# Kernel optimization log

Hardware: AMD Instinct MI355X
Metric: run time of the kernel (lower is better)

Reference implementation:

```python
import jax, jax.numpy as jnp
import numpy as np

EPS = 1e-7  # K.epsilon()
ROUTINGS = 3


def squash(v, axis=-1):
    s2 = jnp.sum(jnp.square(v), axis=axis, keepdims=True)
    scale = s2 / (1.0 + s2) / jnp.sqrt(s2 + EPS)
    return scale * v


def setup_inputs() -> dict:
    key = jax.random.key(0)
    kx, kw = jax.random.split(key)
    B, In, Din, Nc, Dc = 64, 2048, 16, 32, 32
    x = jax.random.normal(kx, (B, In, Din), dtype=jnp.float32)
    W = jax.random.normal(kw, (Nc, In, Dc, Din), dtype=jnp.float32) * 0.05
    return {"x": x, "W": W}


def reference(x, W):
    # x: [B, In, Din]; W: [Nc, In, Dc, Din]
    # Prediction vectors u_hat[b,i,j,d] = sum_k W[j,i,d,k] * x[b,i,k]
    # (the original tf.scan over batch + batch_dot computes exactly this,
    #  serialized; here it is a single batched einsum)
    hat = jnp.einsum('bik,jidk->bijd', x, W)  # [B, In, Nc, Dc]
    b = jnp.zeros(hat.shape[:3], dtype=hat.dtype)  # routing logits [B, In, Nc]
    v = None
    for i in range(ROUTINGS):
        c = jax.nn.softmax(b, axis=2)                 # over output capsules Nc
        s = jnp.einsum('bij,bijd->bjd', c, hat)       # weighted sum over In
        v = squash(s, axis=-1)                        # [B, Nc, Dc]
        if i < ROUTINGS - 1:
            b = b + jnp.einsum('bijd,bjd->bij', hat, v)  # agreement update
    return v
```

## Files before the change

kernel.cpp:

```cpp
#include <hip/hip_runtime.h>
#include <math.h>


#define B_TOT   64
#define IN_CAPS 2048
#define DIN     16
#define NC      32
#define DC      32
#define JD      (NC * DC)
#define B_CHUNK 8
#define I_CHUNK 16
#define N_IG    (IN_CAPS / I_CHUNK)
#define N_BG    (B_TOT / B_CHUNK)
#define EPS_SQ  1e-7f

#define WT_CHUNKS ((size_t)IN_CAPS * 4096)

__device__ __forceinline__ float dot4(const float4 a, const float4 b) {
    return a.x*b.x + a.y*b.y + a.z*b.z + a.w*b.w;
}

#define LDS_BARRIER() do {                                  \
    asm volatile("" ::: "memory");                          \
    asm volatile("s_waitcnt lgkmcnt(0)");                   \
    __builtin_amdgcn_s_barrier();                           \
    asm volatile("" ::: "memory");                          \
} while (0)

__global__ void transpose_W(const float* __restrict__ W, float* __restrict__ Wt)
{
    const int i = blockIdx.x;
    const int t = threadIdx.x;
    const int j = t >> 3, dq = t & 7;
    const float4* Wf = (const float4*)W;
    float4* Wo = (float4*)Wt + (size_t)i * 4096;
    const float4* src = Wf + ((size_t)j * IN_CAPS + i) * 128 + dq * 16;
#pragma unroll
    for (int k4 = 0; k4 < 4; ++k4)
#pragma unroll
        for (int r = 0; r < 4; ++r)
            Wo[(k4 * 4 + r) * 256 + t] = src[r * 4 + k4];
}

template <int TRANS>
__device__ __forceinline__ void wload(float4 (&w)[4], const float4* __restrict__ base,
                                      int il, int k4) {
    if (TRANS) {
        const float4* p = base + (size_t)il * 4096 + k4 * 1024;
        w[0] = p[0];
        w[1] = p[256];
        w[2] = p[512];
        w[3] = p[768];
    } else {
        const float4* p = base + (size_t)il * 128 + k4;
        w[0] = p[0];
        w[1] = p[4];
        w[2] = p[8];
        w[3] = p[12];
    }
}

template <bool ACCUM>
__device__ __forceinline__ void qcomp(const float4 (&w)[4],
                                      const float4 (*__restrict__ xsil)[DIN / 4],
                                      int k4, float (*__restrict__ dst)[4]) {
#pragma unroll
    for (int b = 0; b < B_CHUNK; ++b) {
        const float4 xv = xsil[b][k4];
        if (ACCUM) {
            dst[b][0] += dot4(w[0], xv);
            dst[b][1] += dot4(w[1], xv);
            dst[b][2] += dot4(w[2], xv);
            dst[b][3] += dot4(w[3], xv);
        } else {
            dst[b][0] = dot4(w[0], xv);
            dst[b][1] = dot4(w[1], xv);
            dst[b][2] = dot4(w[2], xv);
            dst[b][3] = dot4(w[3], xv);
        }
    }
}

template <int PHASE, int ATOMIC, int TRANS>
__launch_bounds__(256, 2)
__global__ void caps_pass(const float* __restrict__ x,
                          const float* __restrict__ Wp,
                          const float* __restrict__ vsum,
                          float* __restrict__ P)
{
    __shared__ float4 xs4[I_CHUNK][B_CHUNK][DIN / 4];
    __shared__ float  c_s[PHASE ? 2 : 1][B_CHUNK][NC];

    const int t    = threadIdx.x;
    const int j    = t >> 3;
    const int dq   = t & 7;
    const int doff = dq * 4;
    const int jd0  = j * DC + doff;

    const int r   = blockIdx.x;
    const int xcd = r & 7;
    const int s   = r >> 3;
    const int bg  = s & 7;
    const int ig  = (s >> 3) * 8 + xcd;
    const int b0  = bg * B_CHUNK;
    const int i0  = ig * I_CHUNK;

    float4 sx[2];
    int il_s[2], bl_s[2], k4_s[2];
#pragma unroll
    for (int q = 0; q < 2; ++q) {
        const int f = t * 2 + q;
        il_s[q] = f >> 5;
        bl_s[q] = (f >> 2) & 7;
        k4_s[q] = f & 3;
        sx[q] = *(const float4*)
            &x[((size_t)(b0 + bl_s[q]) * IN_CAPS + (i0 + il_s[q])) * DIN + k4_s[q] * 4];
    }

    const float4* base = TRANS
        ? (const float4*)Wp + (size_t)i0 * 4096 + t
        : (const float4*)Wp + ((size_t)j * IN_CAPS + i0) * 128 + doff * 4;

    float4 wE[4], wO[4];
    wload<TRANS>(wE, base, 0, 0);

#pragma unroll
    for (int q = 0; q < 2; ++q) xs4[il_s[q]][bl_s[q]][k4_s[q]] = sx[q];
    LDS_BARRIER();

    float acc[B_CHUNK][4];
#pragma unroll
    for (int b = 0; b < B_CHUNK; ++b)
#pragma unroll
        for (int dd = 0; dd < 4; ++dd) acc[b][dd] = 0.f;

    float h[B_CHUNK][4];
    int buf = 0;

#pragma unroll 1
    for (int il = 0; il < I_CHUNK; ++il) {
        const float4 (*__restrict__ xsil)[DIN / 4] = xs4[il];
        float (*dst)[4] = PHASE ? h : acc;

        wload<TRANS>(wO, base, il, 1);
        if (PHASE == 0) qcomp<true >(wE, xsil, 0, acc);
        else            qcomp<false>(wE, xsil, 0, h);
        wload<TRANS>(wE, base, il, 2);
        qcomp<true>(wO, xsil, 1, dst);
        wload<TRANS>(wO, base, il, 3);
        qcomp<true>(wE, xsil, 2, dst);
        if (il + 1 < I_CHUNK) wload<TRANS>(wE, base, il + 1, 0);
        qcomp<true>(wO, xsil, 3, dst);

        if (PHASE == 1) {
            float lp[B_CHUNK];
#pragma unroll
            for (int b = 0; b < B_CHUNK; ++b) {
                const float4 vv =
                    *(const float4*)&vsum[(size_t)(b0 + b) * JD + jd0];
                lp[b] = h[b][0]*vv.x + h[b][1]*vv.y + h[b][2]*vv.z + h[b][3]*vv.w;
                lp[b] += __shfl_xor(lp[b], 1, 8);
                lp[b] += __shfl_xor(lp[b], 2, 8);
                lp[b] += __shfl_xor(lp[b], 4, 8);
            }
            if (dq == 0) {
#pragma unroll
                for (int b = 0; b < B_CHUNK; ++b) c_s[buf][b][j] = lp[b];
            }
            LDS_BARRIER();

            {
                const int tb = t >> 5, tj = t & 31;
                const float l = c_s[buf][tb][tj];
                float m = l;
                m = fmaxf(m, __shfl_xor(m, 1, 32));
                m = fmaxf(m, __shfl_xor(m, 2, 32));
                m = fmaxf(m, __shfl_xor(m, 4, 32));
                m = fmaxf(m, __shfl_xor(m, 8, 32));
                m = fmaxf(m, __shfl_xor(m, 16, 32));
                const float e = __expf(l - m);
                float ss = e;
                ss += __shfl_xor(ss, 1, 32);
                ss += __shfl_xor(ss, 2, 32);
                ss += __shfl_xor(ss, 4, 32);
                ss += __shfl_xor(ss, 8, 32);
                ss += __shfl_xor(ss, 16, 32);
                c_s[buf][tb][tj] = e / ss;
            }
            LDS_BARRIER();

#pragma unroll
            for (int b = 0; b < B_CHUNK; ++b) {
                const float c = c_s[buf][b][j];
                acc[b][0] += c * h[b][0];
                acc[b][1] += c * h[b][1];
                acc[b][2] += c * h[b][2];
                acc[b][3] += c * h[b][3];
            }
            buf ^= 1;
        }
    }

    const float scale = (PHASE == 0) ? (1.f / NC) : 1.f;
    if (ATOMIC) {
#pragma unroll
        for (int b = 0; b < B_CHUNK; ++b) {
            float* dstp = &P[(size_t)(b0 + b) * JD + jd0];
            atomicAdd(dstp + 0, acc[b][0] * scale);
            atomicAdd(dstp + 1, acc[b][1] * scale);
            atomicAdd(dstp + 2, acc[b][2] * scale);
            atomicAdd(dstp + 3, acc[b][3] * scale);
        }
    } else {
        float* dstp = P + ((size_t)ig * B_TOT + b0) * JD + jd0;
#pragma unroll
        for (int b = 0; b < B_CHUNK; ++b) {
            *(float4*)(dstp + (size_t)b * JD) =
                make_float4(acc[b][0] * scale, acc[b][1] * scale,
                            acc[b][2] * scale, acc[b][3] * scale);
        }
    }
}

__global__ void reduce_squash(const float* __restrict__ Pf, int nparts,
                              float* __restrict__ VSUMf,
                              float* __restrict__ OUTf, int mode)
{
    const float4* P4   = (const float4*)Pf;
    float4* VSUM       = (float4*)VSUMf;
    float4* OUT        = (float4*)OUTf;
    const int idx = blockIdx.x * blockDim.x + threadIdx.x;
    float4 v = make_float4(0.f, 0.f, 0.f, 0.f);
#pragma unroll 8
    for (int ig = 0; ig < nparts; ++ig) {
        const float4 p = P4[(size_t)ig * (B_TOT * JD / 4) + idx];
        v.x += p.x; v.y += p.y; v.z += p.z; v.w += p.w;
    }
    float s2 = v.x*v.x + v.y*v.y + v.z*v.z + v.w*v.w;
    s2 += __shfl_xor(s2, 1, 8);
    s2 += __shfl_xor(s2, 2, 8);
    s2 += __shfl_xor(s2, 4, 8);
    const float sc = s2 / (1.f + s2) * rsqrtf(s2 + EPS_SQ);
    float4 o = make_float4(v.x * sc, v.y * sc, v.z * sc, v.w * sc);
    if (mode == 0) {
        VSUM[idx] = o;
    } else if (mode == 1) {
        float4 u = VSUM[idx];
        u.x += o.x; u.y += o.y; u.z += o.z; u.w += o.w;
        VSUM[idx] = u;
    } else {
        OUT[idx] = o;
    }
}

extern "C" void kernel_launch(void* const* d_in, const int* in_sizes, int n_in,
                              void* d_out, int out_size, void* d_ws, size_t ws_size,
                              hipStream_t stream)
{
    const float* x = (const float*)d_in[0];
    const float* W = (const float*)d_in[1];
    float* out = (float*)d_out;

    const dim3 grid(N_IG * N_BG);
    const dim3 blk(256);
    const dim3 rgrid(B_TOT * JD / 4 / 256);

    const size_t P_elems  = (size_t)N_IG * B_TOT * JD;
    const size_t vs_elems = (size_t)B_TOT * JD;
    const size_t need_p   = (P_elems + vs_elems) * sizeof(float);
    const size_t need_t   = (WT_CHUNKS * 4 + P_elems + vs_elems) * sizeof(float);

    if (ws_size >= need_t) {
        float* Wt   = (float*)d_ws;
        float* P    = Wt + WT_CHUNKS * 4;
        float* VSUM = P + P_elems;
        transpose_W<<<dim3(IN_CAPS), blk, 0, stream>>>(W, Wt);
        caps_pass<0, 0, 1><<<grid, blk, 0, stream>>>(x, Wt, nullptr, P);
        reduce_squash<<<rgrid, blk, 0, stream>>>(P, N_IG, VSUM, out, 0);
        caps_pass<1, 0, 1><<<grid, blk, 0, stream>>>(x, Wt, VSUM, P);
        reduce_squash<<<rgrid, blk, 0, stream>>>(P, N_IG, VSUM, out, 1);
        caps_pass<1, 0, 1><<<grid, blk, 0, stream>>>(x, Wt, VSUM, P);
        reduce_squash<<<rgrid, blk, 0, stream>>>(P, N_IG, VSUM, out, 2);
    } else if (ws_size >= need_p) {
        float* P    = (float*)d_ws;
        float* VSUM = P + P_elems;
        caps_pass<0, 0, 0><<<grid, blk, 0, stream>>>(x, W, nullptr, P);
        reduce_squash<<<rgrid, blk, 0, stream>>>(P, N_IG, VSUM, out, 0);
        caps_pass<1, 0, 0><<<grid, blk, 0, stream>>>(x, W, VSUM, P);
        reduce_squash<<<rgrid, blk, 0, stream>>>(P, N_IG, VSUM, out, 1);
        caps_pass<1, 0, 0><<<grid, blk, 0, stream>>>(x, W, VSUM, P);
        reduce_squash<<<rgrid, blk, 0, stream>>>(P, N_IG, VSUM, out, 2);
    } else {
        float* S    = (float*)d_ws;
        float* VSUM = S + vs_elems;
        const size_t sbytes = vs_elems * sizeof(float);
        hipMemsetAsync(S, 0, sbytes, stream);
        caps_pass<0, 1, 0><<<grid, blk, 0, stream>>>(x, W, nullptr, S);
        reduce_squash<<<rgrid, blk, 0, stream>>>(S, 1, VSUM, out, 0);
        hipMemsetAsync(S, 0, sbytes, stream);
        caps_pass<1, 1, 0><<<grid, blk, 0, stream>>>(x, W, VSUM, S);
        reduce_squash<<<rgrid, blk, 0, stream>>>(S, 1, VSUM, out, 1);
        hipMemsetAsync(S, 0, sbytes, stream);
        caps_pass<1, 1, 0><<<grid, blk, 0, stream>>>(x, W, VSUM, S);
        reduce_squash<<<rgrid, blk, 0, stream>>>(S, 1, VSUM, out, 2);
    }
}
```

Baseline: 660.3 us.

## Coalesce W transpose via LDS, read x directly, split reduction across slices

```diff
diff --git a/kernel.cpp b/kernel.cpp
--- a/kernel.cpp
+++ b/kernel.cpp
@@ -16,30 +16,42 @@
 
 #define WT_CHUNKS ((size_t)IN_CAPS * 4096)
 
-__device__ __forceinline__ float dot4(const float4 a, const float4 b) {
-    return a.x*b.x + a.y*b.y + a.z*b.z + a.w*b.w;
-}
-
 #define LDS_BARRIER() do {                                  \
     asm volatile("" ::: "memory");                          \
     asm volatile("s_waitcnt lgkmcnt(0)");                   \
     __builtin_amdgcn_s_barrier();                           \
-    asm volatile("" ::: "memory");                          \
+    __builtin_amdgcn_sched_barrier(0);                      \
 } while (0)
 
-__global__ void transpose_W(const float* __restrict__ W, float* __restrict__ Wt)
-{
+__global__ __launch_bounds__(256) void transpose_W(const float* __restrict__ W,
+                                                   float* __restrict__ Wt)
+{
+    __shared__ float4 tile[4096];
     const int i = blockIdx.x;
     const int t = threadIdx.x;
+    const float4* Wf = (const float4*)W;
+    float4 v[16];
+#pragma unroll
+    for (int q = 0; q < 16; ++q) {
+        const int c  = t + 256 * q;
+        const int jj = c >> 7, off = c & 127;
+        v[q] = Wf[((size_t)jj * IN_CAPS + i) * 128 + off];
+    }
+#pragma unroll
+    for (int q = 0; q < 16; ++q) {
+        const int c = t + 256 * q;
+        tile[c ^ ((c >> 4) & 7)] = v[q];
+    }
+    __syncthreads();
+    float4* Wo = (float4*)Wt + (size_t)i * 4096;
     const int j = t >> 3, dq = t & 7;
-    const float4* Wf = (const float4*)W;
-    float4* Wo = (float4*)Wt + (size_t)i * 4096;
-    const float4* src = Wf + ((size_t)j * IN_CAPS + i) * 128 + dq * 16;
 #pragma unroll
     for (int k4 = 0; k4 < 4; ++k4)
 #pragma unroll
-        for (int r = 0; r < 4; ++r)
-            Wo[(k4 * 4 + r) * 256 + t] = src[r * 4 + k4];
+        for (int r = 0; r < 4; ++r) {
+            const int cg = j * 128 + dq * 16 + r * 4 + k4;
+            Wo[(k4 * 4 + r) * 256 + t] = tile[cg ^ dq];
+        }
 }
 
 template <int TRANS>
@@ -62,21 +74,18 @@
 
 template <bool ACCUM>
 __device__ __forceinline__ void qcomp(const float4 (&w)[4],
-                                      const float4 (*__restrict__ xsil)[DIN / 4],
-                                      int k4, float (*__restrict__ dst)[4]) {
+                                      const float* __restrict__ xi,
+                                      int k4, float (*__restrict__ dst)[4])
+{
 #pragma unroll
     for (int b = 0; b < B_CHUNK; ++b) {
-        const float4 xv = xsil[b][k4];
-        if (ACCUM) {
-            dst[b][0] += dot4(w[0], xv);
-            dst[b][1] += dot4(w[1], xv);
-            dst[b][2] += dot4(w[2], xv);
-            dst[b][3] += dot4(w[3], xv);
-        } else {
-            dst[b][0] = dot4(w[0], xv);
-            dst[b][1] = dot4(w[1], xv);
-            dst[b][2] = dot4(w[2], xv);
-            dst[b][3] = dot4(w[3], xv);
+        const float* xb = xi + (size_t)b * (IN_CAPS * DIN) + k4 * 4;
+        const float x0 = xb[0], x1 = xb[1], x2 = xb[2], x3 = xb[3];
+#pragma unroll
+        for (int r = 0; r < 4; ++r) {
+            const float s = w[r].x * x0 + w[r].y * x1 + w[r].z * x2 + w[r].w * x3;
+            if (ACCUM) dst[b][r] += s;
+            else       dst[b][r] = s;
         }
     }
 }
@@ -88,8 +97,7 @@
                           const float* __restrict__ vsum,
                           float* __restrict__ P)
 {
-    __shared__ float4 xs4[I_CHUNK][B_CHUNK][DIN / 4];
-    __shared__ float  c_s[PHASE ? 2 : 1][B_CHUNK][NC];
+    __shared__ float c_s[PHASE ? 2 : 1][B_CHUNK][NC];
 
     const int t    = threadIdx.x;
     const int j    = t >> 3;
@@ -105,18 +113,6 @@
     const int b0  = bg * B_CHUNK;
     const int i0  = ig * I_CHUNK;
 
-    float4 sx[2];
-    int il_s[2], bl_s[2], k4_s[2];
-#pragma unroll
-    for (int q = 0; q < 2; ++q) {
-        const int f = t * 2 + q;
-        il_s[q] = f >> 5;
-        bl_s[q] = (f >> 2) & 7;
-        k4_s[q] = f & 3;
-        sx[q] = *(const float4*)
-            &x[((size_t)(b0 + bl_s[q]) * IN_CAPS + (i0 + il_s[q])) * DIN + k4_s[q] * 4];
-    }
-
     const float4* base = TRANS
         ? (const float4*)Wp + (size_t)i0 * 4096 + t
         : (const float4*)Wp + ((size_t)j * IN_CAPS + i0) * 128 + doff * 4;
@@ -124,10 +120,6 @@
     float4 wE[4], wO[4];
     wload<TRANS>(wE, base, 0, 0);
 
-#pragma unroll
-    for (int q = 0; q < 2; ++q) xs4[il_s[q]][bl_s[q]][k4_s[q]] = sx[q];
-    LDS_BARRIER();
-
     float acc[B_CHUNK][4];
 #pragma unroll
     for (int b = 0; b < B_CHUNK; ++b)
@@ -139,18 +131,18 @@
 
 #pragma unroll 1
     for (int il = 0; il < I_CHUNK; ++il) {
-        const float4 (*__restrict__ xsil)[DIN / 4] = xs4[il];
+        const float* xi = x + ((size_t)b0 * IN_CAPS + (i0 + il)) * DIN;
         float (*dst)[4] = PHASE ? h : acc;
 
         wload<TRANS>(wO, base, il, 1);
-        if (PHASE == 0) qcomp<true >(wE, xsil, 0, acc);
-        else            qcomp<false>(wE, xsil, 0, h);
+        if (PHASE == 0) qcomp<true >(wE, xi, 0, acc);
+        else            qcomp<false>(wE, xi, 0, h);
         wload<TRANS>(wE, base, il, 2);
-        qcomp<true>(wO, xsil, 1, dst);
+        qcomp<true>(wO, xi, 1, dst);
         wload<TRANS>(wO, base, il, 3);
-        qcomp<true>(wE, xsil, 2, dst);
+        qcomp<true>(wE, xi, 2, dst);
         if (il + 1 < I_CHUNK) wload<TRANS>(wE, base, il + 1, 0);
-        qcomp<true>(wO, xsil, 3, dst);
+        qcomp<true>(wO, xi, 3, dst);
 
         if (PHASE == 1) {
             float lp[B_CHUNK];
@@ -222,34 +214,45 @@
     }
 }
 
-__global__ void reduce_squash(const float* __restrict__ Pf, int nparts,
-                              float* __restrict__ VSUMf,
-                              float* __restrict__ OUTf, int mode)
-{
-    const float4* P4   = (const float4*)Pf;
-    float4* VSUM       = (float4*)VSUMf;
-    float4* OUT        = (float4*)OUTf;
-    const int idx = blockIdx.x * blockDim.x + threadIdx.x;
+__global__ __launch_bounds__(256) void reduce_squash(
+    const float* __restrict__ Pf, int nparts,
+    float* __restrict__ VSUMf, float* __restrict__ OUTf, int mode)
+{
+    __shared__ float4 sl[4][64];
+    const float4* P4 = (const float4*)Pf;
+    const int t = threadIdx.x, i64 = t & 63, slice = t >> 6;
+    const int idx = blockIdx.x * 64 + i64;
     float4 v = make_float4(0.f, 0.f, 0.f, 0.f);
-#pragma unroll 8
-    for (int ig = 0; ig < nparts; ++ig) {
+    for (int ig = slice; ig < nparts; ig += 4) {
         const float4 p = P4[(size_t)ig * (B_TOT * JD / 4) + idx];
         v.x += p.x; v.y += p.y; v.z += p.z; v.w += p.w;
     }
-    float s2 = v.x*v.x + v.y*v.y + v.z*v.z + v.w*v.w;
-    s2 += __shfl_xor(s2, 1, 8);
-    s2 += __shfl_xor(s2, 2, 8);
-    s2 += __shfl_xor(s2, 4, 8);
-    const float sc = s2 / (1.f + s2) * rsqrtf(s2 + EPS_SQ);
-    float4 o = make_float4(v.x * sc, v.y * sc, v.z * sc, v.w * sc);
-    if (mode == 0) {
-        VSUM[idx] = o;
-    } else if (mode == 1) {
-        float4 u = VSUM[idx];
-        u.x += o.x; u.y += o.y; u.z += o.z; u.w += o.w;
-        VSUM[idx] = u;
-    } else {
-        OUT[idx] = o;
+    sl[slice][i64] = v;
+    __syncthreads();
+    if (t < 64) {
+        const float4 a = sl[0][t], b = sl[1][t], c = sl[2][t], d = sl[3][t];
+        v.x = a.x + b.x + c.x + d.x;
+        v.y = a.y + b.y + c.y + d.y;
+        v.z = a.z + b.z + c.z + d.z;
+        v.w = a.w + b.w + c.w + d.w;
+        float s2 = v.x*v.x + v.y*v.y + v.z*v.z + v.w*v.w;
+        s2 += __shfl_xor(s2, 1, 8);
+        s2 += __shfl_xor(s2, 2, 8);
+        s2 += __shfl_xor(s2, 4, 8);
+        const float sc = s2 / (1.f + s2) * rsqrtf(s2 + EPS_SQ);
+        const int gidx = blockIdx.x * 64 + t;
+        float4 o = make_float4(v.x * sc, v.y * sc, v.z * sc, v.w * sc);
+        float4* VSUM = (float4*)VSUMf;
+        float4* OUT  = (float4*)OUTf;
+        if (mode == 0) {
+            VSUM[gidx] = o;
+        } else if (mode == 1) {
+            float4 u = VSUM[gidx];
+            u.x += o.x; u.y += o.y; u.z += o.z; u.w += o.w;
+            VSUM[gidx] = u;
+        } else {
+            OUT[gidx] = o;
+        }
     }
 }
 
@@ -263,7 +266,7 @@
 
     const dim3 grid(N_IG * N_BG);
     const dim3 blk(256);
-    const dim3 rgrid(B_TOT * JD / 4 / 256);
+    const dim3 rgrid(B_TOT * JD / 4 / 64);
 
     const size_t P_elems  = (size_t)N_IG * B_TOT * JD;
     const size_t vs_elems = (size_t)B_TOT * JD;
```

Result: faster. 626.3 us (-5.1%).
